# Optimization experiments

Hardware: AMD Instinct MI355X
Metric: run time of the kernel (lower is better)

The kernel has to match this reference:

```python
import jax, jax.numpy as jnp
import numpy as np

HIDDEN = 2048
N_HEADS = 16
N_KV_GROUPS = 4
HEAD_DIM = HIDDEN // N_HEADS  # 128
LATENT = 512
KV_SIZE = HIDDEN * N_KV_GROUPS // N_HEADS  # 512


def setup_inputs() -> dict:
    key = jax.random.key(0)
    ks = jax.random.split(key, 11)
    s = 0.02
    return {
        "hidden_states": jax.random.normal(ks[0], (2, 2048, HIDDEN), dtype=jnp.float32),
        "Wq": jax.random.normal(ks[1], (HIDDEN, HIDDEN), dtype=jnp.float32) * s,
        "bq": jnp.zeros((HIDDEN,), dtype=jnp.float32),
        "Wl": jax.random.normal(ks[2], (HIDDEN, LATENT), dtype=jnp.float32) * s,
        "bl": jnp.zeros((LATENT,), dtype=jnp.float32),
        "Wk": jax.random.normal(ks[3], (LATENT, KV_SIZE), dtype=jnp.float32) * s,
        "bk": jnp.zeros((KV_SIZE,), dtype=jnp.float32),
        "Wv": jax.random.normal(ks[4], (LATENT, KV_SIZE), dtype=jnp.float32) * s,
        "bv": jnp.zeros((KV_SIZE,), dtype=jnp.float32),
        "Wo": jax.random.normal(ks[5], (HIDDEN, HIDDEN), dtype=jnp.float32) * s,
        "bo": jnp.zeros((HIDDEN,), dtype=jnp.float32),
    }


def reference(hidden_states, Wq, bq, Wl, bl, Wk, bk, Wv, bv, Wo, bo):
    B, S, _ = hidden_states.shape
    heads_per_group = N_HEADS // N_KV_GROUPS

    q = hidden_states @ Wq + bq                      # [B,S,H*D]
    latent = hidden_states @ Wl + bl                 # [B,S,L]
    k = latent @ Wk + bk                             # [B,S,G*D]
    v = latent @ Wv + bv

    q = q.reshape(B, S, N_HEADS, HEAD_DIM).transpose(0, 2, 1, 3)        # [B,H,S,D]
    k = k.reshape(B, S, N_KV_GROUPS, HEAD_DIM).transpose(0, 2, 1, 3)    # [B,G,S,D]
    v = v.reshape(B, S, N_KV_GROUPS, HEAD_DIM).transpose(0, 2, 1, 3)

    # repeat_interleave over head dim: group g -> heads [g*hpg, (g+1)*hpg)
    k = jnp.repeat(k, heads_per_group, axis=1)       # [B,H,S,D]
    v = jnp.repeat(v, heads_per_group, axis=1)

    scale = 1.0 / np.sqrt(HEAD_DIM).astype(np.float32)
    scores = jnp.einsum("bhqd,bhkd->bhqk", q, k) * scale
    probs = jax.nn.softmax(scores, axis=-1)          # dropout p=0 (eval) -> identity
    ctx = jnp.einsum("bhqk,bhkd->bhqd", probs, v)    # [B,H,S,D]
    ctx = ctx.transpose(0, 2, 1, 3).reshape(B, S, HIDDEN)
    return ctx @ Wo + bo
```

## Files before the change

kernel.cpp:

```cpp
#include <hip/hip_runtime.h>
#include <stdint.h>


#define DEV static __device__ __forceinline__

using short8  = __attribute__((ext_vector_type(8))) short;
using f32x4   = __attribute__((ext_vector_type(4))) float;
using ushort4v = __attribute__((ext_vector_type(4))) unsigned short;

typedef __attribute__((address_space(1))) void gvoid;
typedef __attribute__((address_space(3))) void lvoid;

DEV unsigned short f2b(float f) {
  unsigned u = __builtin_bit_cast(unsigned, f);
  unsigned r = (u + 0x7fffu + ((u >> 16) & 1u)) >> 16;
  return (unsigned short)r;
}
DEV float b2f(unsigned short s) {
  unsigned u = ((unsigned)s) << 16;
  return __builtin_bit_cast(float, u);
}

DEV unsigned cvtpk(float lo, float hi) {
  unsigned r;
  asm("v_cvt_pk_bf16_f32 %0, %1, %2" : "=v"(r) : "v"(lo), "v"(hi));
  return r;
}

DEV float ex2(float x) { return __builtin_amdgcn_exp2f(x); }

DEV void async16(const void* g, void* l) {
  __builtin_amdgcn_global_load_lds((gvoid*)(uintptr_t)g,
                                   (lvoid*)(uint32_t)(uintptr_t)l, 16, 0, 0);
}

DEV f32x4 mfma16(short8 a, short8 b, f32x4 c) {
  return __builtin_amdgcn_mfma_f32_16x16x32_bf16(a, b, c, 0, 0, 0);
}

__global__ __launch_bounds__(256) void mega_prep(
    const float* __restrict__ h, unsigned short* __restrict__ hb,
    const float* __restrict__ Wq, const float* __restrict__ Wl,
    const float* __restrict__ Wk, const float* __restrict__ Wv,
    const float* __restrict__ Wo,
    unsigned short* __restrict__ WqlT, unsigned short* __restrict__ WkvT,
    unsigned short* __restrict__ WoT,
    const float* __restrict__ bq, const float* __restrict__ bl,
    const float* __restrict__ bk, const float* __restrict__ bv,
    float* __restrict__ bql, float* __restrict__ bkv, float qscale) {
  __shared__ float tile[32][33];
  const int bid = blockIdx.x;
  const int tid = threadIdx.x;

  if (bid < 4096) {
    long i = ((long)bid * 256 + tid) * 8;
    float4 a = *(const float4*)(h + i);
    float4 b = *(const float4*)(h + i + 4);
    short8 o;
    o[0] = (short)f2b(a.x); o[1] = (short)f2b(a.y);
    o[2] = (short)f2b(a.z); o[3] = (short)f2b(a.w);
    o[4] = (short)f2b(b.x); o[5] = (short)f2b(b.y);
    o[6] = (short)f2b(b.z); o[7] = (short)f2b(b.w);
    *(short8*)(hb + i) = o;
    return;
  }

  const float* in; unsigned short* out; int R, C, bx, by; float sc = 1.0f;
  if (bid < 8192) {
    int l = bid - 4096; in = Wq; out = WqlT; R = 2048; C = 2048;
    bx = l & 63; by = l >> 6; sc = qscale;
  } else if (bid < 9216) {
    int l = bid - 8192; in = Wl; out = WqlT + 2048 * 2048; R = 2048; C = 512;
    bx = l & 15; by = l >> 4;
  } else if (bid < 9472) {
    int l = bid - 9216; in = Wk; out = WkvT; R = 512; C = 512;
    bx = l & 15; by = l >> 4;
  } else if (bid < 9728) {
    int l = bid - 9472; in = Wv; out = WkvT + 262144; R = 512; C = 512;
    bx = l & 15; by = l >> 4;
  } else if (bid < 13824) {
    int l = bid - 9728; in = Wo; out = WoT; R = 2048; C = 2048;
    bx = l & 63; by = l >> 6;
  } else {
    for (int t = tid; t < 2560; t += 256)
      bql[t] = (t < 2048) ? bq[t] * qscale : bl[t - 2048];
    for (int t = tid; t < 1024; t += 256)
      bkv[t] = (t < 512) ? bk[t] : bv[t - 512];
    return;
  }

  int bc = bx * 32, br = by * 32;
  int tx = tid & 31, ty0 = tid >> 5;
#pragma unroll
  for (int ty = ty0; ty < 32; ty += 8)
    tile[ty][tx] = in[(size_t)(br + ty) * C + bc + tx] * sc;
  __syncthreads();
#pragma unroll
  for (int ty = ty0; ty < 32; ty += 8)
    out[(size_t)(bc + ty) * R + br + tx] = f2b(tile[tx][ty]);
}

__global__ __launch_bounds__(256) void gemm_kv(
    const unsigned short* __restrict__ A,
    const unsigned short* __restrict__ Bt,
    const float* __restrict__ bias,
    unsigned short* __restrict__ kvb,
    unsigned short* __restrict__ vtb) {
  const int K = 512, lda = 2560;
  __shared__ unsigned short As[128 * 32];
  __shared__ unsigned short Bs[128 * 32];
  int tid = threadIdx.x;
  int lane = tid & 63, wave = tid >> 6;
  int wr = wave >> 1, wc = wave & 1;
  int lq = lane & 15, grp = lane >> 4;
  int brow = blockIdx.y * 128, bcol = blockIdx.x * 128;

  f32x4 acc[4][4] = {};

  for (int k0 = 0; k0 < K; k0 += 32) {
    {
      int e0 = tid * 8;
      int r0 = e0 >> 5, c0 = e0 & 31;
      async16(A + (size_t)(brow + r0) * lda + k0 + c0, As + e0);
      async16(Bt + (size_t)(bcol + r0) * K + k0 + c0, Bs + e0);
      int e1 = (256 + tid) * 8;
      int r1 = e1 >> 5, c1 = e1 & 31;
      async16(A + (size_t)(brow + r1) * lda + k0 + c1, As + e1);
      async16(Bt + (size_t)(bcol + r1) * K + k0 + c1, Bs + e1);
    }
    __syncthreads();

    short8 af[4], bf[4];
#pragma unroll
    for (int m = 0; m < 4; m++)
      af[m] = *(const short8*)(As + (wr * 64 + m * 16 + lq) * 32 + grp * 8);
#pragma unroll
    for (int n = 0; n < 4; n++)
      bf[n] = *(const short8*)(Bs + (wc * 64 + n * 16 + lq) * 32 + grp * 8);
#pragma unroll
    for (int m = 0; m < 4; m++)
#pragma unroll
      for (int n = 0; n < 4; n++)
        acc[m][n] = mfma16(af[m], bf[n], acc[m][n]);
    __syncthreads();
  }

#pragma unroll
  for (int n = 0; n < 4; n++) {
    int col = bcol + wc * 64 + n * 16 + lq;
    float bv = bias[col];
    if (col < 512) {
#pragma unroll
      for (int m = 0; m < 4; m++) {
#pragma unroll
        for (int r = 0; r < 4; r++) {
          int row = brow + wr * 64 + m * 16 + grp * 4 + r;
          kvb[(size_t)row * 1024 + col] = f2b(acc[m][n][r] + bv);
        }
      }
    } else {
      int vc = col - 512;
#pragma unroll
      for (int m = 0; m < 4; m++) {
        int row0 = brow + wr * 64 + m * 16 + grp * 4;
        int b = row0 >> 11, s0 = row0 & 2047;
        ushort4v pk;
        pk[0] = f2b(acc[m][n][0] + bv);
        pk[1] = f2b(acc[m][n][1] + bv);
        pk[2] = f2b(acc[m][n][2] + bv);
        pk[3] = f2b(acc[m][n][3] + bv);
        *(ushort4v*)(vtb + ((size_t)(b * 512 + vc)) * 2048 + s0) = pk;
      }
    }
  }
}

template <int OUT_F32>
__global__ __launch_bounds__(512, 1) void gemm_8ph(
    const unsigned short* __restrict__ A, const unsigned short* __restrict__ Bt,
    const float* __restrict__ bias, void* __restrict__ Cout,
    int M, int N, int K, float scale) {
  __shared__ __align__(1024) unsigned short L[2][32768];
  const int tid = threadIdx.x, lane = tid & 63, wave = tid >> 6;
  const int lq = lane & 15, grp = lane >> 4;
  const int wr = wave >> 2, wc = wave & 3;

  const int gx = gridDim.x;
  int nwg = gx * gridDim.y;
  int bid = blockIdx.y * gx + blockIdx.x;
  int wgid = (bid & 7) * (nwg >> 3) + (bid >> 3);
  int bx = wgid % gx, by = wgid / gx;
  const int brow = by * 256, bcol = bx * 256;

  const unsigned short* srcA[2];
  const unsigned short* srcB[2];
  unsigned short* dstA[2];
  unsigned short* dstB[2];
#pragma unroll
  for (int j = 0; j < 2; j++) {
    int f = wave + j * 8, kk = f & 1, fi = f >> 1;
    int awr = fi >> 2, aml = fi & 3;
    srcA[j] = A + (size_t)(brow + (awr * 8 + aml) * 16 + lq) * K + kk * 32 + grp * 8;
    dstA[j] = &L[0][0] + f * 512 + lane * 8;
    int bwc = fi >> 1, bnl = fi & 1;
    srcB[j] = Bt + (size_t)(bcol + (bwc * 4 + bnl) * 16 + lq) * K + kk * 32 + grp * 8;
    dstB[j] = &L[0][0] + 16384 + f * 512 + lane * 8;
  }
  auto stgA = [&](int p, int mh, int k0) {
#pragma unroll
    for (int j = 0; j < 2; j++)
      async16(srcA[j] + (size_t)mh * 64 * K + k0, dstA[j] + p * 32768 + mh * 8192);
  };
  auto stgB = [&](int p, int nh, int k0) {
#pragma unroll
    for (int j = 0; j < 2; j++)
      async16(srcB[j] + (size_t)nh * 32 * K + k0, dstB[j] + p * 32768 + nh * 8192);
  };
  auto ldAf = [&](int p, int mh, int ml, int kk) -> short8 {
    return *(const short8*)(&L[0][0] + p * 32768 + mh * 8192 +
                            ((wr * 4 + ml) * 2 + kk) * 512 + lane * 8);
  };
  auto ldBf = [&](int p, int nh, int nl, int kk) -> short8 {
    return *(const short8*)(&L[0][0] + p * 32768 + 16384 + nh * 8192 +
                            ((wc * 2 + nl) * 2 + kk) * 512 + lane * 8);
  };

  f32x4 acc[8][4] = {};
  short8 af[4][2], bf0[2][2], bf1[2][2];
  const int NT = K >> 6;

  stgA(0, 0, 0); stgB(0, 0, 0); stgB(0, 1, 0); stgA(0, 1, 0);
  asm volatile("s_waitcnt vmcnt(4)" ::: "memory");
  __builtin_amdgcn_s_barrier();

  for (int T = 0; T < NT; ++T) {
    const int cur = T & 1, nxt = cur ^ 1;
    const bool pf = (T + 1 < NT);
    const int k1 = (T + 1) << 6;

#pragma unroll
    for (int ml = 0; ml < 4; ml++) {
      af[ml][0] = ldAf(cur, 0, ml, 0);
      af[ml][1] = ldAf(cur, 0, ml, 1);
    }
#pragma unroll
    for (int nl = 0; nl < 2; nl++) {
      bf0[nl][0] = ldBf(cur, 0, nl, 0);
      bf0[nl][1] = ldBf(cur, 0, nl, 1);
    }
    if (pf) stgA(nxt, 0, k1);
    __builtin_amdgcn_s_setprio(1);
#pragma unroll
    for (int ml = 0; ml < 4; ml++)
#pragma unroll
      for (int nl = 0; nl < 2; nl++) {
        acc[ml][nl] = mfma16(af[ml][0], bf0[nl][0], acc[ml][nl]);
        acc[ml][nl] = mfma16(af[ml][1], bf0[nl][1], acc[ml][nl]);
      }
    __builtin_amdgcn_s_setprio(0);
    if (pf) asm volatile("s_waitcnt vmcnt(4)" ::: "memory");
    else    asm volatile("s_waitcnt vmcnt(2)" ::: "memory");
    __builtin_amdgcn_s_barrier();

#pragma unroll
    for (int nl = 0; nl < 2; nl++) {
      bf1[nl][0] = ldBf(cur, 1, nl, 0);
      bf1[nl][1] = ldBf(cur, 1, nl, 1);
    }
    if (pf) stgB(nxt, 0, k1);
    __builtin_amdgcn_s_setprio(1);
#pragma unroll
    for (int ml = 0; ml < 4; ml++)
#pragma unroll
      for (int nl = 0; nl < 2; nl++) {
        acc[ml][2 + nl] = mfma16(af[ml][0], bf1[nl][0], acc[ml][2 + nl]);
        acc[ml][2 + nl] = mfma16(af[ml][1], bf1[nl][1], acc[ml][2 + nl]);
      }
    __builtin_amdgcn_s_setprio(0);
    if (pf) asm volatile("s_waitcnt vmcnt(4)" ::: "memory");
    else    asm volatile("s_waitcnt vmcnt(0)" ::: "memory");
    __builtin_amdgcn_s_barrier();

#pragma unroll
    for (int ml = 0; ml < 4; ml++) {
      af[ml][0] = ldAf(cur, 1, ml, 0);
      af[ml][1] = ldAf(cur, 1, ml, 1);
    }
    if (pf) stgB(nxt, 1, k1);
    __builtin_amdgcn_s_setprio(1);
#pragma unroll
    for (int ml = 0; ml < 4; ml++)
#pragma unroll
      for (int nl = 0; nl < 2; nl++) {
        acc[4 + ml][nl] = mfma16(af[ml][0], bf0[nl][0], acc[4 + ml][nl]);
        acc[4 + ml][nl] = mfma16(af[ml][1], bf0[nl][1], acc[4 + ml][nl]);
      }
    __builtin_amdgcn_s_setprio(0);
    __builtin_amdgcn_s_barrier();

    if (pf) stgA(nxt, 1, k1);
    __builtin_amdgcn_s_setprio(1);
#pragma unroll
    for (int ml = 0; ml < 4; ml++)
#pragma unroll
      for (int nl = 0; nl < 2; nl++) {
        acc[4 + ml][2 + nl] = mfma16(af[ml][0], bf1[nl][0], acc[4 + ml][2 + nl]);
        acc[4 + ml][2 + nl] = mfma16(af[ml][1], bf1[nl][1], acc[4 + ml][2 + nl]);
      }
    __builtin_amdgcn_s_setprio(0);
    if (pf) asm volatile("s_waitcnt vmcnt(4)" ::: "memory");
    __builtin_amdgcn_s_barrier();
  }

#pragma unroll
  for (int mh = 0; mh < 2; mh++)
#pragma unroll
    for (int ml = 0; ml < 4; ml++)
#pragma unroll
      for (int nh = 0; nh < 2; nh++)
#pragma unroll
        for (int nl = 0; nl < 2; nl++) {
          int col = bcol + wc * 64 + (nh * 2 + nl) * 16 + lq;
          float bv = bias[col];
          f32x4 a = acc[mh * 4 + ml][nh * 2 + nl];
#pragma unroll
          for (int r = 0; r < 4; r++) {
            int row = brow + wr * 128 + (mh * 4 + ml) * 16 + grp * 4 + r;
            float v = (a[r] + bv) * scale;
            if (OUT_F32)
              ((float*)Cout)[(size_t)row * N + col] = v;
            else
              ((unsigned short*)Cout)[(size_t)row * N + col] = f2b(v);
          }
        }
}

__global__ __launch_bounds__(256, 2) void attn_kernel(
    const unsigned short* __restrict__ q,
    const unsigned short* __restrict__ kv,
    const unsigned short* __restrict__ vt,
    unsigned short* __restrict__ ctx) {
  __shared__ unsigned short KV[2][32][512];
  const int lane = threadIdx.x & 63, wave = threadIdx.x >> 6;
  const int lq = lane & 15, grp = lane >> 4;
  const int bid = blockIdx.x;
  const int combo = bid & 7;
  const int slot = bid >> 3;
  const int b = combo >> 2, g = combo & 3;
  const int h = g * 4 + (slot >> 4);
  const int qbase = (slot & 15) * 128 + wave * 32;

  short8 qf[2][4];
#pragma unroll
  for (int qs = 0; qs < 2; qs++) {
    const unsigned short* qp =
        q + ((size_t)(b * 2048 + qbase + qs * 16 + lq)) * 2560 + h * 128 + grp * 8;
#pragma unroll
    for (int c = 0; c < 4; c++) qf[qs][c] = *(const short8*)(qp + c * 32);
  }

  f32x4 o[2][8] = {};
  float lsum[2] = {0.f, 0.f};
  const float C = 20.0f;

  const int kvperm = (lq >> 2) * 8 + (lq & 3);
  const unsigned short* kB = kv + (size_t)b * 2048 * 1024 + g * 128 + grp * 8;
  const unsigned short* vB =
      vt + ((size_t)((b * 4 + g) * 128 + lq)) * 2048 + grp * 8;
  const int fbase = wave * 8;
  unsigned short* dstb = &KV[0][fbase][0] + lane * 8;

  auto stage = [&](int bn, int kv0) {
    unsigned short* dst = dstb + bn * 16384;
    if (fbase < 16) {
#pragma unroll
      for (int j = 0; j < 8; j++) {
        int f = fbase + j, t = f >> 2, c = f & 3;
        const unsigned short* src =
            kB + (size_t)(kv0 + (t >> 1) * 32 + (t & 1) * 4 + kvperm) * 1024 + c * 32;
        async16(src, dst + j * 512);
      }
    } else {
#pragma unroll
      for (int j = 0; j < 8; j++) {
        int f = fbase - 16 + j, d0 = f >> 1, u = f & 1;
        const unsigned short* src = vB + (size_t)(d0 * 16) * 2048 + kv0 + u * 32;
        async16(src, dst + j * 512);
      }
    }
  };

  stage(0, 0);
  int buf = 0;
  for (int it = 0; it < 32; ++it) {
    __syncthreads();
    if (it < 31) stage(buf ^ 1, (it + 1) * 64);
    const unsigned short* Kb = &KV[buf][0][0] + lane * 8;

    f32x4 s[2][4] = {};
    __builtin_amdgcn_s_setprio(1);
#pragma unroll
    for (int c = 0; c < 4; c++) {
      short8 kf0 = *(const short8*)(Kb + (0 + c) * 512);
      short8 kf1 = *(const short8*)(Kb + (4 + c) * 512);
      short8 kf2 = *(const short8*)(Kb + (8 + c) * 512);
      short8 kf3 = *(const short8*)(Kb + (12 + c) * 512);
#pragma unroll
      for (int qs = 0; qs < 2; qs++) {
        s[qs][0] = mfma16(kf0, qf[qs][c], s[qs][0]);
        s[qs][1] = mfma16(kf1, qf[qs][c], s[qs][1]);
        s[qs][2] = mfma16(kf2, qf[qs][c], s[qs][2]);
        s[qs][3] = mfma16(kf3, qf[qs][c], s[qs][3]);
      }
    }
    __builtin_amdgcn_s_setprio(0);

    short8 pf[2][2];
#pragma unroll
    for (int qs = 0; qs < 2; qs++) {
      float ps = 0.f;
      union { short8 v; unsigned w[4]; } pk0, pk1;
#pragma unroll
      for (int t = 0; t < 4; t++) {
        float e0 = ex2(s[qs][t][0] - C);
        float e1 = ex2(s[qs][t][1] - C);
        float e2 = ex2(s[qs][t][2] - C);
        float e3 = ex2(s[qs][t][3] - C);
        ps += (e0 + e1) + (e2 + e3);
        unsigned w0 = cvtpk(e0, e1), w1 = cvtpk(e2, e3);
        if (t == 0) { pk0.w[0] = w0; pk0.w[1] = w1; }
        else if (t == 1) { pk0.w[2] = w0; pk0.w[3] = w1; }
        else if (t == 2) { pk1.w[0] = w0; pk1.w[1] = w1; }
        else { pk1.w[2] = w0; pk1.w[3] = w1; }
      }
      lsum[qs] += ps;
      pf[qs][0] = pk0.v;
      pf[qs][1] = pk1.v;
    }

    const unsigned short* Vb = Kb + 16 * 512;
    __builtin_amdgcn_s_setprio(1);
#pragma unroll
    for (int d0 = 0; d0 < 8; d0++) {
      short8 v0 = *(const short8*)(Vb + (d0 * 2 + 0) * 512);
      short8 v1 = *(const short8*)(Vb + (d0 * 2 + 1) * 512);
#pragma unroll
      for (int qs = 0; qs < 2; qs++) {
        o[qs][d0] = mfma16(pf[qs][0], v0, o[qs][d0]);
        o[qs][d0] = mfma16(pf[qs][1], v1, o[qs][d0]);
      }
    }
    __builtin_amdgcn_s_setprio(0);
    buf ^= 1;
  }

  unsigned short* cp = ctx + ((size_t)(b * 2048 + qbase)) * 2048 + h * 128;
#pragma unroll
  for (int qs = 0; qs < 2; qs++) {
    float l = lsum[qs];
    l += __shfl_xor(l, 16);
    l += __shfl_xor(l, 32);
    float ri = 1.0f / l;
    float r0 = __shfl(ri, grp * 4 + 0), r1 = __shfl(ri, grp * 4 + 1);
    float r2 = __shfl(ri, grp * 4 + 2), r3 = __shfl(ri, grp * 4 + 3);
#pragma unroll
    for (int d0 = 0; d0 < 8; d0++) {
      int col = d0 * 16 + lq;
      cp[(size_t)(qs * 16 + grp * 4 + 0) * 2048 + col] = f2b(o[qs][d0][0] * r0);
      cp[(size_t)(qs * 16 + grp * 4 + 1) * 2048 + col] = f2b(o[qs][d0][1] * r1);
      cp[(size_t)(qs * 16 + grp * 4 + 2) * 2048 + col] = f2b(o[qs][d0][2] * r2);
      cp[(size_t)(qs * 16 + grp * 4 + 3) * 2048 + col] = f2b(o[qs][d0][3] * r3);
    }
  }
}

extern "C" void kernel_launch(void* const* d_in, const int* in_sizes, int n_in,
                              void* d_out, int out_size, void* d_ws, size_t ws_size,
                              hipStream_t stream) {
  const float* h  = (const float*)d_in[0];
  const float* Wq = (const float*)d_in[1];
  const float* bq = (const float*)d_in[2];
  const float* Wl = (const float*)d_in[3];
  const float* bl = (const float*)d_in[4];
  const float* Wk = (const float*)d_in[5];
  const float* bk = (const float*)d_in[6];
  const float* Wv = (const float*)d_in[7];
  const float* bv = (const float*)d_in[8];
  const float* Wo = (const float*)d_in[9];
  const float* bo = (const float*)d_in[10];
  float* out = (float*)d_out;

  const int M = 4096;

  char* w = (char*)d_ws;
  auto take = [&](size_t elems) {
    void* p = (void*)w;
    w += (elems * 2 + 255) & ~(size_t)255;
    return (unsigned short*)p;
  };
  unsigned short* hb   = take(8388608);
  unsigned short* WqlT = take(5242880);
  unsigned short* WkvT = take(524288);
  unsigned short* WoT  = take(4194304);
  unsigned short* qlat = take(10485760);
  unsigned short* kvb  = take(4194304);
  unsigned short* vtb  = take(2097152);
  unsigned short* ctx  = take(8388608);
  float* bql = (float*)take(2560);
  float* bkv = (float*)take(1024);

  const float scale = 0.08838834764831845f * 1.4426950408889634f;

  mega_prep<<<13825, 256, 0, stream>>>(h, hb, Wq, Wl, Wk, Wv, Wo,
                                       WqlT, WkvT, WoT,
                                       bq, bl, bk, bv, bql, bkv, scale);

  gemm_8ph<0><<<dim3(10, 16), 512, 0, stream>>>(hb, WqlT, bql, qlat, M, 2560, 2048, 1.0f);
  gemm_kv<<<dim3(8, 32), 256, 0, stream>>>(qlat + 2048, WkvT, bkv, kvb, vtb);

  attn_kernel<<<512, 256, 0, stream>>>(qlat, kvb, vtb, ctx);

  gemm_8ph<1><<<dim3(8, 16), 512, 0, stream>>>(ctx, WoT, bo, out, M, 2048, 2048, 1.0f);
}
```

Measured before the change: 237.3 us.

## Split-K the output projection GEMM with atomic accumulation and bias pre-init

The output projection GEMM now splits K in two across a third grid dimension. This doubles the workgroup count so more CUs are busy, and each half accumulates into the fp32 output with atomic adds. A new small kernel first writes the bias into the output buffer. The cost is an extra launch, an extra full-output write, atomic traffic in the epilogue, and a summation order that is no longer deterministic.

```diff
diff --git a/kernel.cpp b/kernel.cpp
--- a/kernel.cpp
+++ b/kernel.cpp
@@ -36,6 +36,14 @@
 
 DEV f32x4 mfma16(short8 a, short8 b, f32x4 c) {
   return __builtin_amdgcn_mfma_f32_16x16x32_bf16(a, b, c, 0, 0, 0);
+}
+
+__global__ __launch_bounds__(256) void init_out(
+    float* __restrict__ out, const float* __restrict__ bo) {
+  int i = (blockIdx.x * 256 + threadIdx.x) * 4;
+  int col = i & 2047;
+  float4 b = *(const float4*)(bo + col);
+  *(float4*)(out + i) = b;
 }
 
 __global__ __launch_bounds__(256) void mega_prep(
@@ -175,15 +183,16 @@
   }
 }
 
-template <int OUT_F32>
+template <int MODE>
 __global__ __launch_bounds__(512, 1) void gemm_8ph(
     const unsigned short* __restrict__ A, const unsigned short* __restrict__ Bt,
     const float* __restrict__ bias, void* __restrict__ Cout,
-    int M, int N, int K, float scale) {
+    int M, int N, int Kst, int KS, float scale) {
   __shared__ __align__(1024) unsigned short L[2][32768];
   const int tid = threadIdx.x, lane = tid & 63, wave = tid >> 6;
   const int lq = lane & 15, grp = lane >> 4;
   const int wr = wave >> 2, wc = wave & 3;
+  const int kbase = blockIdx.z * KS;
 
   const int gx = gridDim.x;
   int nwg = gx * gridDim.y;
@@ -200,21 +209,21 @@
   for (int j = 0; j < 2; j++) {
     int f = wave + j * 8, kk = f & 1, fi = f >> 1;
     int awr = fi >> 2, aml = fi & 3;
-    srcA[j] = A + (size_t)(brow + (awr * 8 + aml) * 16 + lq) * K + kk * 32 + grp * 8;
+    srcA[j] = A + (size_t)(brow + (awr * 8 + aml) * 16 + lq) * Kst + kk * 32 + grp * 8;
     dstA[j] = &L[0][0] + f * 512 + lane * 8;
     int bwc = fi >> 1, bnl = fi & 1;
-    srcB[j] = Bt + (size_t)(bcol + (bwc * 4 + bnl) * 16 + lq) * K + kk * 32 + grp * 8;
+    srcB[j] = Bt + (size_t)(bcol + (bwc * 4 + bnl) * 16 + lq) * Kst + kk * 32 + grp * 8;
     dstB[j] = &L[0][0] + 16384 + f * 512 + lane * 8;
   }
   auto stgA = [&](int p, int mh, int k0) {
 #pragma unroll
     for (int j = 0; j < 2; j++)
-      async16(srcA[j] + (size_t)mh * 64 * K + k0, dstA[j] + p * 32768 + mh * 8192);
+      async16(srcA[j] + (size_t)mh * 64 * Kst + k0, dstA[j] + p * 32768 + mh * 8192);
   };
   auto stgB = [&](int p, int nh, int k0) {
 #pragma unroll
     for (int j = 0; j < 2; j++)
-      async16(srcB[j] + (size_t)nh * 32 * K + k0, dstB[j] + p * 32768 + nh * 8192);
+      async16(srcB[j] + (size_t)nh * 32 * Kst + k0, dstB[j] + p * 32768 + nh * 8192);
   };
   auto ldAf = [&](int p, int mh, int ml, int kk) -> short8 {
     return *(const short8*)(&L[0][0] + p * 32768 + mh * 8192 +
@@ -227,16 +236,16 @@
 
   f32x4 acc[8][4] = {};
   short8 af[4][2], bf0[2][2], bf1[2][2];
-  const int NT = K >> 6;
-
-  stgA(0, 0, 0); stgB(0, 0, 0); stgB(0, 1, 0); stgA(0, 1, 0);
+  const int NT = KS >> 6;
+
+  stgA(0, 0, kbase); stgB(0, 0, kbase); stgB(0, 1, kbase); stgA(0, 1, kbase);
   asm volatile("s_waitcnt vmcnt(4)" ::: "memory");
   __builtin_amdgcn_s_barrier();
 
   for (int T = 0; T < NT; ++T) {
     const int cur = T & 1, nxt = cur ^ 1;
     const bool pf = (T + 1 < NT);
-    const int k1 = (T + 1) << 6;
+    const int k1 = kbase + ((T + 1) << 6);
 
 #pragma unroll
     for (int ml = 0; ml < 4; ml++) {
@@ -321,16 +330,20 @@
 #pragma unroll
         for (int nl = 0; nl < 2; nl++) {
           int col = bcol + wc * 64 + (nh * 2 + nl) * 16 + lq;
-          float bv = bias[col];
           f32x4 a = acc[mh * 4 + ml][nh * 2 + nl];
-#pragma unroll
-          for (int r = 0; r < 4; r++) {
-            int row = brow + wr * 128 + (mh * 4 + ml) * 16 + grp * 4 + r;
-            float v = (a[r] + bv) * scale;
-            if (OUT_F32)
-              ((float*)Cout)[(size_t)row * N + col] = v;
-            else
-              ((unsigned short*)Cout)[(size_t)row * N + col] = f2b(v);
+          if (MODE == 0) {
+            float bv = bias[col];
+#pragma unroll
+            for (int r = 0; r < 4; r++) {
+              int row = brow + wr * 128 + (mh * 4 + ml) * 16 + grp * 4 + r;
+              ((unsigned short*)Cout)[(size_t)row * N + col] = f2b((a[r] + bv) * scale);
+            }
+          } else {
+#pragma unroll
+            for (int r = 0; r < 4; r++) {
+              int row = brow + wr * 128 + (mh * 4 + ml) * 16 + grp * 4 + r;
+              unsafeAtomicAdd(&((float*)Cout)[(size_t)row * N + col], a[r] * scale);
+            }
           }
         }
 }
@@ -515,10 +528,11 @@
                                        WqlT, WkvT, WoT,
                                        bq, bl, bk, bv, bql, bkv, scale);
 
-  gemm_8ph<0><<<dim3(10, 16), 512, 0, stream>>>(hb, WqlT, bql, qlat, M, 2560, 2048, 1.0f);
+  gemm_8ph<0><<<dim3(10, 16, 1), 512, 0, stream>>>(hb, WqlT, bql, qlat, M, 2560, 2048, 2048, 1.0f);
   gemm_kv<<<dim3(8, 32), 256, 0, stream>>>(qlat + 2048, WkvT, bkv, kvb, vtb);
 
   attn_kernel<<<512, 256, 0, stream>>>(qlat, kvb, vtb, ctx);
 
-  gemm_8ph<1><<<dim3(8, 16), 512, 0, stream>>>(ctx, WoT, bo, out, M, 2048, 2048, 1.0f);
-}
+  init_out<<<8192, 256, 0, stream>>>(out, bo);
+  gemm_8ph<2><<<dim3(8, 16, 2), 512, 0, stream>>>(ctx, WoT, nullptr, out, M, 2048, 2048, 1024, 1.0f);
+}
```

After: 261.4 us. 10.2% more time.
